# Kernel tuning notes

Hardware: AMD Instinct MI355X
Metric: run time of the kernel (lower is better)

The kernel has to match this reference:

```python
import jax, jax.numpy as jnp
import numpy as np

CDIM = 256  # part_size for energy_pooling_mask


def setup_inputs() -> dict:
    key = jax.random.key(0)
    ks = jax.random.split(key, 6)
    B, T, IDIM, HDIM, ODIM = 8, 2048, 512, 2048, 512
    x = jax.random.normal(ks[0], (B, T, IDIM), dtype=jnp.float32)
    mask_prev = jax.random.randint(ks[1], (B, T, HDIM), 0, 2, dtype=jnp.int32)
    W_enc = jax.random.normal(ks[2], (HDIM, IDIM), dtype=jnp.float32) * 0.02
    b_enc = jax.random.normal(ks[3], (HDIM,), dtype=jnp.float32) * 0.02
    W_dec = jax.random.normal(ks[4], (ODIM, HDIM), dtype=jnp.float32) * 0.02
    b_dec = jax.random.normal(ks[5], (ODIM,), dtype=jnp.float32) * 0.02
    return {"x": x, "mask_prev": mask_prev, "W_enc": W_enc, "b_enc": b_enc,
            "W_dec": W_dec, "b_dec": b_dec}


def _energy_pooling_mask(h, part_size):
    # topk over channel (last) dim of h^2; share=True -> k = 2*part_size
    B, T, H = h.shape
    k2 = 2 * part_size
    _, idx = jax.lax.top_k(h * h, k2)            # [B, T, 2c] unique indices
    idx_f = idx.reshape(B * T, k2)
    rows = jnp.arange(B * T)[:, None]
    base = jnp.zeros((B * T, H), dtype=h.dtype)
    # sum of one-hots over unique indices == scatter-set of 1.0
    mask_share = base.at[rows, idx_f].set(1.0).reshape(B, T, H)
    mask_cur = base.at[rows, idx_f[:, :part_size]].set(1.0).reshape(B, T, H)
    return mask_cur, mask_share


def reference(x, mask_prev, W_enc, b_enc, W_dec, b_dec):
    # encoder: Linear(idim -> hdim)
    h = jnp.einsum('bti,hi->bth', x, W_enc) + b_enc
    # hidden_exclude_activation with mask_prev given:
    # h[mask_prev.bool()] = 0
    mp = mask_prev.astype(h.dtype)
    h = jnp.where(mp > 0, jnp.zeros((), h.dtype), h)
    mask_cur, mask_cur_share = _energy_pooling_mask(h, CDIM)
    mask_prev_new = mp + mask_cur
    # h.masked_fill(~mask_cur_share.bool(), 0)
    h = h * mask_cur_share
    # decoder_src: Linear(hdim -> odim)
    out = jnp.einsum('bth,oh->bto', h, W_dec) + b_dec
    return out, mask_prev_new
```

## Files before the change

kernel.cpp:

```cpp
#include <hip/hip_runtime.h>
#include <hip/hip_bf16.h>

typedef __attribute__((ext_vector_type(8))) __bf16 bf16x8;
typedef __attribute__((ext_vector_type(4))) float f32x4;

#define MDIM 16384
#define HDIM 2048
#define IDIM 512
#define ODIM 512
#define CAP 768

static __device__ __forceinline__ unsigned short f2bf(float f) {
  unsigned int u = __float_as_uint(f);
  unsigned int r = (u + 0x7fffu + ((u >> 16) & 1u)) >> 16;
  return (unsigned short)r;
}

__global__ void cvt_bf16_kernel(const float* __restrict__ src,
                                unsigned short* __restrict__ dst, int n) {
  int i = (blockIdx.x * 256 + threadIdx.x) * 4;
  if (i >= n) return;
  float4 v = *(const float4*)(src + i);
  unsigned int a = (unsigned int)f2bf(v.x) | ((unsigned int)f2bf(v.y) << 16);
  unsigned int b = (unsigned int)f2bf(v.z) | ((unsigned int)f2bf(v.w) << 16);
  uint2 st; st.x = a; st.y = b;
  *(uint2*)(dst + i) = st;
}

__global__ __launch_bounds__(256) void gemm1_kernel(
    const float* __restrict__ x,
    const float* __restrict__ wenc,
    const float* __restrict__ benc,
    float* __restrict__ h) {
  __shared__ __align__(16) float As[16][132];
  __shared__ __align__(16) float Bs[16][132];
  const int t = threadIdx.x;
  const int tx = t & 15, ty = t >> 4;
  const int m0 = blockIdx.y * 128;
  const int n0 = blockIdx.x * 128;
  const int r0 = t >> 2;
  const int k4 = (t & 3) * 4;

  const float* pa0 = x + (size_t)(m0 + r0) * IDIM + k4;
  const float* pa1 = x + (size_t)(m0 + 64 + r0) * IDIM + k4;
  const float* pb0 = wenc + (size_t)(n0 + r0) * IDIM + k4;
  const float* pb1 = wenc + (size_t)(n0 + 64 + r0) * IDIM + k4;

  float acc[8][8];
#pragma unroll
  for (int i = 0; i < 8; ++i)
#pragma unroll
    for (int j = 0; j < 8; ++j) acc[i][j] = 0.f;

  float4 a0 = *(const float4*)(pa0);
  float4 a1 = *(const float4*)(pa1);
  float4 b0 = *(const float4*)(pb0);
  float4 b1 = *(const float4*)(pb1);

  for (int kt = 0; kt < IDIM; kt += 16) {
    __syncthreads();
#pragma unroll
    for (int j = 0; j < 4; ++j) {
      As[k4 + j][r0]      = ((const float*)&a0)[j];
      As[k4 + j][64 + r0] = ((const float*)&a1)[j];
      Bs[k4 + j][r0]      = ((const float*)&b0)[j];
      Bs[k4 + j][64 + r0] = ((const float*)&b1)[j];
    }
    __syncthreads();
    if (kt + 16 < IDIM) {
      a0 = *(const float4*)(pa0 + kt + 16);
      a1 = *(const float4*)(pa1 + kt + 16);
      b0 = *(const float4*)(pb0 + kt + 16);
      b1 = *(const float4*)(pb1 + kt + 16);
    }
#pragma unroll
    for (int k = 0; k < 16; ++k) {
      float4 av0 = *(const float4*)&As[k][ty * 4];
      float4 av1 = *(const float4*)&As[k][64 + ty * 4];
      float4 bv0 = *(const float4*)&Bs[k][tx * 4];
      float4 bv1 = *(const float4*)&Bs[k][64 + tx * 4];
      float am[8] = {av0.x, av0.y, av0.z, av0.w, av1.x, av1.y, av1.z, av1.w};
      float bm[8] = {bv0.x, bv0.y, bv0.z, bv0.w, bv1.x, bv1.y, bv1.z, bv1.w};
#pragma unroll
      for (int i = 0; i < 8; ++i)
#pragma unroll
        for (int j = 0; j < 8; ++j) acc[i][j] += am[i] * bm[j];
    }
  }
  float4 be0 = *(const float4*)(benc + n0 + tx * 4);
  float4 be1 = *(const float4*)(benc + n0 + 64 + tx * 4);
  float bb[8] = {be0.x, be0.y, be0.z, be0.w, be1.x, be1.y, be1.z, be1.w};
#pragma unroll
  for (int i = 0; i < 8; ++i) {
    int m = m0 + ((i < 4) ? (ty * 4 + i) : (64 + ty * 4 + (i - 4)));
    float* hrow = h + (size_t)m * HDIM + n0;
    float4 s0 = {acc[i][0] + bb[0], acc[i][1] + bb[1], acc[i][2] + bb[2], acc[i][3] + bb[3]};
    float4 s1 = {acc[i][4] + bb[4], acc[i][5] + bb[5], acc[i][6] + bb[6], acc[i][7] + bb[7]};
    *(float4*)(hrow + tx * 4) = s0;
    *(float4*)(hrow + 64 + tx * 4) = s1;
  }
}

__global__ __launch_bounds__(256) void select_kernel(
    float* __restrict__ hbuf,
    const int* __restrict__ maskp,
    unsigned short* __restrict__ hs) {
  const int row = blockIdx.x;
  const int t = threadIdx.x;
  const int lane = t & 63;
  const int w = t >> 6;
  __shared__ int hist[4096];
  __shared__ unsigned int cand512[CAP];
  __shared__ unsigned int cand256[CAP];
  __shared__ int scal[16];
  __shared__ int n512, n256;

  float* hrow = hbuf + (size_t)row * HDIM;
  const int* mrow = maskp + (size_t)row * HDIM;
  float hv[8];
  *(float4*)&hv[0] = *(const float4*)(hrow + t * 8);
  *(float4*)&hv[4] = *(const float4*)(hrow + t * 8 + 4);
  int4 mp0 = *(const int4*)(mrow + t * 8);
  int4 mp1 = *(const int4*)(mrow + t * 8 + 4);
  int mm[8] = {mp0.x, mp0.y, mp0.z, mp0.w, mp1.x, mp1.y, mp1.z, mp1.w};
#pragma unroll
  for (int i = 0; i < 8; ++i) hv[i] = (mm[i] > 0) ? 0.f : hv[i];
  unsigned int key[8];
#pragma unroll
  for (int i = 0; i < 8; ++i) key[i] = __float_as_uint(hv[i] * hv[i]);

#pragma unroll
  for (int i = 0; i < 16; ++i) hist[t + i * 256] = 0;
  if (t == 0) {
    n512 = 0; n256 = 0;
    scal[0] = 0; scal[1] = 0x40000000;
    scal[2] = 0; scal[3] = 0x40000000;
  }
  __syncthreads();
#pragma unroll
  for (int i = 0; i < 8; ++i)
    if (key[i]) atomicAdd(&hist[key[i] >> 20], 1);
  __syncthreads();

  if (w == 0) {
    const int base = lane * 64;
    int s = 0;
#pragma unroll
    for (int i = 0; i < 64; i += 4) {
      int4 hh = *(const int4*)&hist[base + i];
      s += hh.x + hh.y + hh.z + hh.w;
    }
    int rs = s;
#pragma unroll
    for (int d = 1; d < 64; d <<= 1) {
      int o = __shfl_down(rs, d, 64);
      rs += (lane + d < 64) ? o : 0;
    }
    int c = rs - s;
    for (int i = 60; i >= 0; i -= 4) {
      int4 hh = *(const int4*)&hist[base + i];
      int q[4] = {hh.x, hh.y, hh.z, hh.w};
#pragma unroll
      for (int j = 3; j >= 0; --j) {
        int hc = q[j];
        if (c < 512 && c + hc >= 512) { scal[0] = base + i + j; scal[1] = 512 - c; }
        if (c < 256 && c + hc >= 256) { scal[2] = base + i + j; scal[3] = 256 - c; }
        c += hc;
      }
    }
  }
  __syncthreads();
  const int b512 = scal[0], b256 = scal[2];
#pragma unroll
  for (int i = 0; i < 8; ++i) {
    if (key[i]) {
      int bin = (int)(key[i] >> 20);
      if (bin == b512) { int p = atomicAdd(&n512, 1); if (p < CAP) cand512[p] = key[i]; }
      if (bin == b256) { int p = atomicAdd(&n256, 1); if (p < CAP) cand256[p] = key[i]; }
    }
  }
  __syncthreads();

  if (w < 2) {
    const unsigned int bb = (unsigned int)scal[w * 2];
    const int r = scal[w * 2 + 1];
    const unsigned int* cand = w ? cand256 : cand512;
    int C = w ? n256 : n512;
    C = (C < CAP) ? C : CAP;
    unsigned int v = 0;
    if (r <= C) {
      v = bb << 20;
      for (int bit = 19; bit >= 0; --bit) {
        unsigned int cth = v | (1u << bit);
        int cnt = 0;
        for (int p = lane; p < C; p += 64) cnt += (cand[p] >= cth) ? 1 : 0;
#pragma unroll
        for (int d = 1; d < 64; d <<= 1) cnt += __shfl_xor(cnt, d, 64);
        if (cnt >= r) v = cth;
      }
    }
    if (lane == 0) scal[4 + w] = (int)v;
  }
  __syncthreads();
  const unsigned int v512 = (unsigned int)scal[4];
  const unsigned int v256 = (unsigned int)scal[5];

  int g = 0;
#pragma unroll
  for (int i = 0; i < 8; ++i) {
    g += (key[i] > v512) ? 1 : 0;
    g += (key[i] > v256) ? (1 << 16) : 0;
  }
#pragma unroll
  for (int d = 1; d < 64; d <<= 1) g += __shfl_xor(g, d, 64);
  if (lane == 0) scal[8 + w] = g;
  __syncthreads();
  g = scal[8] + scal[9] + scal[10] + scal[11];
  const int r512 = 512 - (g & 0xffff);
  const int r256 = 256 - (g >> 16);

  int tc = 0;
#pragma unroll
  for (int i = 0; i < 8; ++i) {
    tc += (key[i] == v512) ? 1 : 0;
    tc += (key[i] == v256) ? (1 << 16) : 0;
  }
  int sc = tc;
#pragma unroll
  for (int d = 1; d < 64; d <<= 1) {
    int o = __shfl_up(sc, d, 64);
    if (lane >= d) sc += o;
  }
  if (lane == 63) scal[12 + w] = sc;
  __syncthreads();
  int excl = sc - tc;
  for (int i = 0; i < w; ++i) excl += scal[12 + i];
  int run512 = excl & 0xffff;
  int run256 = (excl >> 16) & 0xffff;

  float mpn[8];
  unsigned int hb[4];
#pragma unroll
  for (int i = 0; i < 8; ++i) {
    bool share, cur;
    if (key[i] > v512) share = true;
    else if (key[i] == v512) { share = (run512 < r512); run512++; }
    else share = false;
    if (key[i] > v256) cur = true;
    else if (key[i] == v256) { cur = (run256 < r256); run256++; }
    else cur = false;
    mpn[i] = (float)mm[i] + (cur ? 1.0f : 0.0f);
    unsigned short bbits = f2bf(share ? hv[i] : 0.0f);
    if (i & 1) hb[i >> 1] |= ((unsigned int)bbits << 16);
    else hb[i >> 1] = (unsigned int)bbits;
  }
  float4 s0 = {mpn[0], mpn[1], mpn[2], mpn[3]};
  float4 s1 = {mpn[4], mpn[5], mpn[6], mpn[7]};
  *(float4*)(hrow + t * 8) = s0;
  *(float4*)(hrow + t * 8 + 4) = s1;
  uint4 hstore = {hb[0], hb[1], hb[2], hb[3]};
  *(uint4*)(hs + (size_t)row * HDIM + t * 8) = hstore;
}

__global__ __launch_bounds__(256) void gemm2_kernel(
    const unsigned short* __restrict__ A,
    const unsigned short* __restrict__ B,
    const float* __restrict__ bdec,
    float* __restrict__ out) {
  __shared__ __align__(16) __bf16 As[128 * 32];
  __shared__ __align__(16) __bf16 Bs[128 * 32];
  const int t = threadIdx.x;
  const int lane = t & 63;
  const int w = t >> 6;
  const int wm = w >> 1, wn = w & 1;
  const int m0 = blockIdx.y * 128;
  const int n0 = blockIdx.x * 128;
  const int r = t >> 2;
  const int k8 = (t & 3) * 8;

  f32x4 acc[4][4];
#pragma unroll
  for (int i = 0; i < 4; ++i)
#pragma unroll
    for (int j = 0; j < 4; ++j) acc[i][j] = (f32x4){0.f, 0.f, 0.f, 0.f};

  const int la = lane & 15;
  const int kq = (lane >> 4) * 8;

  for (int kt = 0; kt < HDIM; kt += 32) {
    uint4 a0 = *(const uint4*)(A + (size_t)(m0 + r) * HDIM + kt + k8);
    uint4 a1 = *(const uint4*)(A + (size_t)(m0 + 64 + r) * HDIM + kt + k8);
    uint4 b0 = *(const uint4*)(B + (size_t)(n0 + r) * HDIM + kt + k8);
    uint4 b1 = *(const uint4*)(B + (size_t)(n0 + 64 + r) * HDIM + kt + k8);
    __syncthreads();
    *(uint4*)&As[r * 32 + k8] = a0;
    *(uint4*)&As[(64 + r) * 32 + k8] = a1;
    *(uint4*)&Bs[r * 32 + k8] = b0;
    *(uint4*)&Bs[(64 + r) * 32 + k8] = b1;
    __syncthreads();
    bf16x8 af[4], bg[4];
#pragma unroll
    for (int mi = 0; mi < 4; ++mi)
      af[mi] = *(const bf16x8*)&As[(wm * 64 + mi * 16 + la) * 32 + kq];
#pragma unroll
    for (int ni = 0; ni < 4; ++ni)
      bg[ni] = *(const bf16x8*)&Bs[(wn * 64 + ni * 16 + la) * 32 + kq];
#pragma unroll
    for (int mi = 0; mi < 4; ++mi)
#pragma unroll
      for (int ni = 0; ni < 4; ++ni)
        acc[mi][ni] = __builtin_amdgcn_mfma_f32_16x16x32_bf16(
            af[mi], bg[ni], acc[mi][ni], 0, 0, 0);
  }
  const int rq = (lane >> 4) * 4;
#pragma unroll
  for (int mi = 0; mi < 4; ++mi) {
#pragma unroll
    for (int ni = 0; ni < 4; ++ni) {
      int n = n0 + wn * 64 + ni * 16 + la;
      float bd = bdec[n];
#pragma unroll
      for (int rr = 0; rr < 4; ++rr) {
        int m = m0 + wm * 64 + mi * 16 + rq + rr;
        out[(size_t)m * ODIM + n] = acc[mi][ni][rr] + bd;
      }
    }
  }
}

extern "C" void kernel_launch(void* const* d_in, const int* in_sizes, int n_in,
                              void* d_out, int out_size, void* d_ws, size_t ws_size,
                              hipStream_t stream) {
  const float* x = (const float*)d_in[0];
  const int* mask_prev = (const int*)d_in[1];
  const float* W_enc = (const float*)d_in[2];
  const float* b_enc = (const float*)d_in[3];
  const float* W_dec = (const float*)d_in[4];
  const float* b_dec = (const float*)d_in[5];

  float* out = (float*)d_out;
  float* hbuf = out + (size_t)MDIM * ODIM;
  unsigned short* hs = (unsigned short*)d_ws;
  unsigned short* wdec = hs + (size_t)MDIM * HDIM;

  cvt_bf16_kernel<<<dim3((ODIM * HDIM) / (256 * 4)), dim3(256), 0, stream>>>(
      W_dec, wdec, ODIM * HDIM);
  gemm1_kernel<<<dim3(HDIM / 128, MDIM / 128), dim3(256), 0, stream>>>(
      x, W_enc, b_enc, hbuf);
  select_kernel<<<dim3(MDIM), dim3(256), 0, stream>>>(hbuf, mask_prev, hs);
  gemm2_kernel<<<dim3(ODIM / 128, MDIM / 128), dim3(256), 0, stream>>>(
      hs, wdec, b_dec, out);
}
```

Before: 855.9 us.

## Double-buffer gemm1 LDS tiles, convert W_dec inline in gemm2, halve gemm2 M tile

gemm1 now keeps two LDS buffers, so the next k-tile is written while the current one is consumed and only one barrier is needed per iteration. The separate W_dec fp32-to-bf16 conversion kernel is removed; gemm2 reads fp32 W_dec and converts it to bf16 in registers on every tile load. gemm2's M tile drops from 128 to 64, which doubles the block count. The inline conversion multiplies fp32 weight traffic and conversion work across every M block, in exchange for one fewer launch and more parallelism in gemm2.

Result: no change. 870.0 us (+1.7%).

```diff
diff --git a/kernel.cpp b/kernel.cpp
--- a/kernel.cpp
+++ b/kernel.cpp
@@ -15,16 +15,8 @@
   unsigned int r = (u + 0x7fffu + ((u >> 16) & 1u)) >> 16;
   return (unsigned short)r;
 }
-
-__global__ void cvt_bf16_kernel(const float* __restrict__ src,
-                                unsigned short* __restrict__ dst, int n) {
-  int i = (blockIdx.x * 256 + threadIdx.x) * 4;
-  if (i >= n) return;
-  float4 v = *(const float4*)(src + i);
-  unsigned int a = (unsigned int)f2bf(v.x) | ((unsigned int)f2bf(v.y) << 16);
-  unsigned int b = (unsigned int)f2bf(v.z) | ((unsigned int)f2bf(v.w) << 16);
-  uint2 st; st.x = a; st.y = b;
-  *(uint2*)(dst + i) = st;
+static __device__ __forceinline__ unsigned int pk2bf(float a, float b) {
+  return (unsigned int)f2bf(a) | ((unsigned int)f2bf(b) << 16);
 }
 
 __global__ __launch_bounds__(256) void gemm1_kernel(
@@ -32,8 +24,8 @@
     const float* __restrict__ wenc,
     const float* __restrict__ benc,
     float* __restrict__ h) {
-  __shared__ __align__(16) float As[16][132];
-  __shared__ __align__(16) float Bs[16][132];
+  __shared__ __align__(16) float As[2][16][132];
+  __shared__ __align__(16) float Bs[2][16][132];
   const int t = threadIdx.x;
   const int tx = t & 15, ty = t >> 4;
   const int m0 = blockIdx.y * 128;
@@ -56,18 +48,19 @@
   float4 a1 = *(const float4*)(pa1);
   float4 b0 = *(const float4*)(pb0);
   float4 b1 = *(const float4*)(pb1);
+#pragma unroll
+  for (int j = 0; j < 4; ++j) {
+    As[0][k4 + j][r0]      = ((const float*)&a0)[j];
+    As[0][k4 + j][64 + r0] = ((const float*)&a1)[j];
+    Bs[0][k4 + j][r0]      = ((const float*)&b0)[j];
+    Bs[0][k4 + j][64 + r0] = ((const float*)&b1)[j];
+  }
+  int p = 0;
 
   for (int kt = 0; kt < IDIM; kt += 16) {
     __syncthreads();
-#pragma unroll
-    for (int j = 0; j < 4; ++j) {
-      As[k4 + j][r0]      = ((const float*)&a0)[j];
-      As[k4 + j][64 + r0] = ((const float*)&a1)[j];
-      Bs[k4 + j][r0]      = ((const float*)&b0)[j];
-      Bs[k4 + j][64 + r0] = ((const float*)&b1)[j];
-    }
-    __syncthreads();
-    if (kt + 16 < IDIM) {
+    const bool more = (kt + 16 < IDIM);
+    if (more) {
       a0 = *(const float4*)(pa0 + kt + 16);
       a1 = *(const float4*)(pa1 + kt + 16);
       b0 = *(const float4*)(pb0 + kt + 16);
@@ -75,10 +68,10 @@
     }
 #pragma unroll
     for (int k = 0; k < 16; ++k) {
-      float4 av0 = *(const float4*)&As[k][ty * 4];
-      float4 av1 = *(const float4*)&As[k][64 + ty * 4];
-      float4 bv0 = *(const float4*)&Bs[k][tx * 4];
-      float4 bv1 = *(const float4*)&Bs[k][64 + tx * 4];
+      float4 av0 = *(const float4*)&As[p][k][ty * 4];
+      float4 av1 = *(const float4*)&As[p][k][64 + ty * 4];
+      float4 bv0 = *(const float4*)&Bs[p][k][tx * 4];
+      float4 bv1 = *(const float4*)&Bs[p][k][64 + tx * 4];
       float am[8] = {av0.x, av0.y, av0.z, av0.w, av1.x, av1.y, av1.z, av1.w};
       float bm[8] = {bv0.x, bv0.y, bv0.z, bv0.w, bv1.x, bv1.y, bv1.z, bv1.w};
 #pragma unroll
@@ -86,6 +79,16 @@
 #pragma unroll
         for (int j = 0; j < 8; ++j) acc[i][j] += am[i] * bm[j];
     }
+    if (more) {
+#pragma unroll
+      for (int j = 0; j < 4; ++j) {
+        As[p ^ 1][k4 + j][r0]      = ((const float*)&a0)[j];
+        As[p ^ 1][k4 + j][64 + r0] = ((const float*)&a1)[j];
+        Bs[p ^ 1][k4 + j][r0]      = ((const float*)&b0)[j];
+        Bs[p ^ 1][k4 + j][64 + r0] = ((const float*)&b1)[j];
+      }
+    }
+    p ^= 1;
   }
   float4 be0 = *(const float4*)(benc + n0 + tx * 4);
   float4 be1 = *(const float4*)(benc + n0 + 64 + tx * 4);
@@ -264,23 +267,23 @@
 
 __global__ __launch_bounds__(256) void gemm2_kernel(
     const unsigned short* __restrict__ A,
-    const unsigned short* __restrict__ B,
+    const float* __restrict__ Wd,
     const float* __restrict__ bdec,
     float* __restrict__ out) {
-  __shared__ __align__(16) __bf16 As[128 * 32];
+  __shared__ __align__(16) __bf16 As[64 * 32];
   __shared__ __align__(16) __bf16 Bs[128 * 32];
   const int t = threadIdx.x;
   const int lane = t & 63;
   const int w = t >> 6;
   const int wm = w >> 1, wn = w & 1;
-  const int m0 = blockIdx.y * 128;
+  const int m0 = blockIdx.y * 64;
   const int n0 = blockIdx.x * 128;
   const int r = t >> 2;
   const int k8 = (t & 3) * 8;
 
-  f32x4 acc[4][4];
-#pragma unroll
-  for (int i = 0; i < 4; ++i)
+  f32x4 acc[2][4];
+#pragma unroll
+  for (int i = 0; i < 2; ++i)
 #pragma unroll
     for (int j = 0; j < 4; ++j) acc[i][j] = (f32x4){0.f, 0.f, 0.f, 0.f};
 
@@ -289,24 +292,31 @@
 
   for (int kt = 0; kt < HDIM; kt += 32) {
     uint4 a0 = *(const uint4*)(A + (size_t)(m0 + r) * HDIM + kt + k8);
-    uint4 a1 = *(const uint4*)(A + (size_t)(m0 + 64 + r) * HDIM + kt + k8);
-    uint4 b0 = *(const uint4*)(B + (size_t)(n0 + r) * HDIM + kt + k8);
-    uint4 b1 = *(const uint4*)(B + (size_t)(n0 + 64 + r) * HDIM + kt + k8);
+    const float* w0p = Wd + (size_t)(n0 + r) * HDIM + kt + k8;
+    const float* w1p = Wd + (size_t)(n0 + 64 + r) * HDIM + kt + k8;
+    float4 w0a = *(const float4*)(w0p);
+    float4 w0b = *(const float4*)(w0p + 4);
+    float4 w1a = *(const float4*)(w1p);
+    float4 w1b = *(const float4*)(w1p + 4);
+    uint4 b0, b1;
+    b0.x = pk2bf(w0a.x, w0a.y); b0.y = pk2bf(w0a.z, w0a.w);
+    b0.z = pk2bf(w0b.x, w0b.y); b0.w = pk2bf(w0b.z, w0b.w);
+    b1.x = pk2bf(w1a.x, w1a.y); b1.y = pk2bf(w1a.z, w1a.w);
+    b1.z = pk2bf(w1b.x, w1b.y); b1.w = pk2bf(w1b.z, w1b.w);
     __syncthreads();
     *(uint4*)&As[r * 32 + k8] = a0;
-    *(uint4*)&As[(64 + r) * 32 + k8] = a1;
     *(uint4*)&Bs[r * 32 + k8] = b0;
     *(uint4*)&Bs[(64 + r) * 32 + k8] = b1;
     __syncthreads();
-    bf16x8 af[4], bg[4];
-#pragma unroll
-    for (int mi = 0; mi < 4; ++mi)
-      af[mi] = *(const bf16x8*)&As[(wm * 64 + mi * 16 + la) * 32 + kq];
+    bf16x8 af[2], bg[4];
+#pragma unroll
+    for (int mi = 0; mi < 2; ++mi)
+      af[mi] = *(const bf16x8*)&As[(wm * 32 + mi * 16 + la) * 32 + kq];
 #pragma unroll
     for (int ni = 0; ni < 4; ++ni)
       bg[ni] = *(const bf16x8*)&Bs[(wn * 64 + ni * 16 + la) * 32 + kq];
 #pragma unroll
-    for (int mi = 0; mi < 4; ++mi)
+    for (int mi = 0; mi < 2; ++mi)
 #pragma unroll
       for (int ni = 0; ni < 4; ++ni)
         acc[mi][ni] = __builtin_amdgcn_mfma_f32_16x16x32_bf16(
@@ -314,14 +324,14 @@
   }
   const int rq = (lane >> 4) * 4;
 #pragma unroll
-  for (int mi = 0; mi < 4; ++mi) {
+  for (int mi = 0; mi < 2; ++mi) {
 #pragma unroll
     for (int ni = 0; ni < 4; ++ni) {
       int n = n0 + wn * 64 + ni * 16 + la;
       float bd = bdec[n];
 #pragma unroll
       for (int rr = 0; rr < 4; ++rr) {
-        int m = m0 + wm * 64 + mi * 16 + rq + rr;
+        int m = m0 + wm * 32 + mi * 16 + rq + rr;
         out[(size_t)m * ODIM + n] = acc[mi][ni][rr] + bd;
       }
     }
@@ -341,13 +351,10 @@
   float* out = (float*)d_out;
   float* hbuf = out + (size_t)MDIM * ODIM;
   unsigned short* hs = (unsigned short*)d_ws;
-  unsigned short* wdec = hs + (size_t)MDIM * HDIM;
-
-  cvt_bf16_kernel<<<dim3((ODIM * HDIM) / (256 * 4)), dim3(256), 0, stream>>>(
-      W_dec, wdec, ODIM * HDIM);
+
   gemm1_kernel<<<dim3(HDIM / 128, MDIM / 128), dim3(256), 0, stream>>>(
       x, W_enc, b_enc, hbuf);
   select_kernel<<<dim3(MDIM), dim3(256), 0, stream>>>(hbuf, mask_prev, hs);
-  gemm2_kernel<<<dim3(ODIM / 128, MDIM / 128), dim3(256), 0, stream>>>(
-      hs, wdec, b_dec, out);
-}
+  gemm2_kernel<<<dim3(ODIM / 128, MDIM / 64), dim3(256), 0, stream>>>(
+      hs, W_dec, b_dec, out);
+}
```
